# Kernel optimization log

Measured on AMD Instinct MI355X. Metric: run time of the kernel, lower is better.

The kernel has to match this reference:

```python
import jax, jax.numpy as jnp
import numpy as np

N = 8192
HID = 64
TAU = 0.8
LAMBDA = 0.5
POS_DENSITY = 0.005


def setup_inputs() -> dict:
    key = jax.random.key(0)
    k1, k2, k3, k4, k5, k6, k7 = jax.random.split(key, 7)
    x1 = jax.random.normal(k1, (N, HID), dtype=jnp.float32)
    x2 = jax.random.normal(k2, (N, HID), dtype=jnp.float32)
    # xavier_uniform with gain=1.414 for square [HID, HID] linears
    limit = 1.414 * np.sqrt(6.0 / (HID + HID))
    W1 = jax.random.uniform(k3, (HID, HID), dtype=jnp.float32, minval=-limit, maxval=limit)
    b1 = jnp.zeros((HID,), dtype=jnp.float32)
    W2 = jax.random.uniform(k4, (HID, HID), dtype=jnp.float32, minval=-limit, maxval=limit)
    b2 = jnp.zeros((HID,), dtype=jnp.float32)
    pm = (jax.random.uniform(k5, (N, N), dtype=jnp.float32) < POS_DENSITY).astype(jnp.float32)
    positive_matrix = jnp.maximum(pm, jnp.eye(N, dtype=jnp.float32))
    return {"x1": x1, "x2": x2, "W1": W1, "b1": b1, "W2": W2, "b2": b2,
            "positive_matrix": positive_matrix}


def _project(x, W1, b1, W2, b2):
    # nn.Linear(hidden, hidden) -> ELU -> nn.Linear(hidden, hidden)
    h = jax.nn.elu(x @ W1.T + b1)
    return h @ W2.T + b2


def _l2norm(z, eps=1e-12):
    # F.normalize(p=2, dim=1): x / max(||x||, eps)
    n = jnp.linalg.norm(z, axis=-1, keepdims=True)
    return z / jnp.maximum(n, eps)


def _sim(z1, z2, tau):
    return jnp.exp((_l2norm(z1) @ _l2norm(z2).T) / tau)  # [N, N]


def _masked_loss(sim_mat, pos):
    row = sim_mat / (jnp.sum(sim_mat, axis=-1, keepdims=True) + 1e-8)
    return -jnp.log(jnp.sum(row * pos, axis=-1) + 1e-8).mean()


def reference(x1, x2, W1, b1, W2, b2, positive_matrix):
    z1 = _project(x1, W1, b1, W2, b2)
    z2 = _project(x2, W1, b1, W2, b2)
    sc_mp = _sim(z1, z2, TAU)
    mp_sc = _sim(z2, z1, TAU)
    sc_loss = _masked_loss(sc_mp, positive_matrix)
    mp_loss = _masked_loss(mp_sc, positive_matrix)
    return sc_loss * LAMBDA + mp_loss * (1.0 - LAMBDA)
```

## Files before the change

kernel.cpp:

```cpp
#include <hip/hip_runtime.h>
#include <hip/hip_bf16.h>

#define N 8192
#define HID 64
#define JC 8

typedef __attribute__((ext_vector_type(4))) float f32x4;
typedef __attribute__((ext_vector_type(8))) __bf16 bf16x8;

__device__ __forceinline__ void gload_lds16(const void* g, float* l) {
  __builtin_amdgcn_global_load_lds(
      (const __attribute__((address_space(1))) void*)g,
      (__attribute__((address_space(3))) void*)l, 16, 0, 0);
}

__global__ __launch_bounds__(256) void proj_kernel(
    const float* __restrict__ x1, const float* __restrict__ x2,
    const float* __restrict__ W1, const float* __restrict__ b1,
    const float* __restrict__ W2, const float* __restrict__ b2,
    __bf16* __restrict__ Z1h, __bf16* __restrict__ Z2h,
    float* __restrict__ stats)
{
  __shared__ __align__(16) float w1s[64*68];
  __shared__ __align__(16) float w2s[64*68];
  __shared__ __align__(16) float xs[4][64];
  __shared__ __align__(16) float hs[4][64];

  const int tid  = threadIdx.x;
  const int lane = tid & 63;
  const int w    = tid >> 6;

  int gtid = blockIdx.x * 256 + tid;
  if (gtid < 4*N) stats[gtid] = 0.f;

  for (int idx = tid; idx < 64*64; idx += 256) {
    int j = idx >> 6, k = idx & 63;
    w1s[j*68+k] = W1[idx];
    w2s[j*68+k] = W2[idx];
  }
  __syncthreads();

  const float bias1 = b1[lane];
  const float bias2 = b2[lane];

  const int wave_global = blockIdx.x * 4 + w;
  #pragma unroll 1
  for (int it = 0; it < 4; ++it) {
    int R = wave_global * 4 + it;
    const float* src; __bf16* dst;
    if (R < N) { src = x1 + (size_t)R*HID;      dst = Z1h + (size_t)R*HID; }
    else       { src = x2 + (size_t)(R-N)*HID;  dst = Z2h + (size_t)(R-N)*HID; }

    float xv = src[lane];
    xs[w][lane] = xv;
    float acc = bias1;
    #pragma unroll
    for (int qq = 0; qq < 16; ++qq) {
      f32x4 xq = *(const f32x4*)&xs[w][qq*4];
      f32x4 wq = *(const f32x4*)&w1s[lane*68 + qq*4];
      acc += xq.x*wq.x + xq.y*wq.y + xq.z*wq.z + xq.w*wq.w;
    }
    float h = acc > 0.f ? acc : expm1f(acc);
    hs[w][lane] = h;
    float acc2 = bias2;
    #pragma unroll
    for (int qq = 0; qq < 16; ++qq) {
      f32x4 hq = *(const f32x4*)&hs[w][qq*4];
      f32x4 wq = *(const f32x4*)&w2s[lane*68 + qq*4];
      acc2 += hq.x*wq.x + hq.y*wq.y + hq.z*wq.z + hq.w*wq.w;
    }
    float z = acc2;
    float ss = z*z;
    #pragma unroll
    for (int m = 1; m < 64; m <<= 1) ss += __shfl_xor(ss, m);
    float inv = 1.0f / fmaxf(sqrtf(ss), 1e-12f);
    dst[lane] = (__bf16)(z * inv);
  }
}

__global__ __launch_bounds__(256, 4) void sim_kernel(
    const __bf16* __restrict__ Z1h, const __bf16* __restrict__ Z2h,
    const float* __restrict__ pos,
    float* __restrict__ rowsum1, float* __restrict__ num1,
    float* __restrict__ rowsum2, float* __restrict__ num2)
{
  __shared__ __align__(16) float zs1[2][2048];
  __shared__ __align__(16) float zs2[2][2048];

  const int tid  = threadIdx.x;
  const int lane = tid & 63;
  const int w    = tid >> 6;
  const int r16  = lane & 15;
  const int q    = lane >> 4;

  const int bi  = blockIdx.x / JC;
  const int jc  = blockIdx.x % JC;
  const int i0  = bi*64 + w*16;

  const __bf16* z1r = Z1h + (size_t)(i0 + r16)*HID + q*8;
  const __bf16* z2r = Z2h + (size_t)(i0 + r16)*HID + q*8;
  const bf16x8 a1lo = *(const bf16x8*)(z1r);
  const bf16x8 a1hi = *(const bf16x8*)(z1r + 32);
  const bf16x8 a2lo = *(const bf16x8*)(z2r);
  const bf16x8 a2hi = *(const bf16x8*)(z2r + 32);

  float s1 = 0.f, n1 = 0.f, s2 = 0.f, n2 = 0.f;

  const int jbeg = jc * (N/JC);
  const float Cexp = 1.8033688011112042f;
  const float* prow = pos + (size_t)(i0 + r16)*N + q*4;

  f32x4 PA0, PA1, PA2, PA3, PB0, PB1, PB2, PB3;

#define STAGEZ(BUF, JJ) { \
    const int r8 = lane >> 3; \
    const int sl = (lane & 7) ^ r8; \
    gload_lds16(Z1h + (size_t)((JJ) + w*16     + r8)*HID + sl*8, &zs1[BUF][(w*16    )*32]); \
    gload_lds16(Z1h + (size_t)((JJ) + w*16 + 8 + r8)*HID + sl*8, &zs1[BUF][(w*16 + 8)*32]); \
    gload_lds16(Z2h + (size_t)((JJ) + w*16     + r8)*HID + sl*8, &zs2[BUF][(w*16    )*32]); \
    gload_lds16(Z2h + (size_t)((JJ) + w*16 + 8 + r8)*HID + sl*8, &zs2[BUF][(w*16 + 8)*32]); \
  }

#define LOADPOS(P, JJ) { \
    P##0 = *(const f32x4*)(prow + (JJ)); \
    P##1 = *(const f32x4*)(prow + (JJ) + 16); \
    P##2 = *(const f32x4*)(prow + (JJ) + 32); \
    P##3 = *(const f32x4*)(prow + (JJ) + 48); \
  }

#define COMPC(BUF, C, CC, PV) { \
    const int R  = (CC) + (C)*16 + r16; \
    const int sw = r16 & 7; \
    bf16x8 b2lo = *(const bf16x8*)&zs2[BUF][R*32 + ((q    ) ^ sw)*4]; \
    bf16x8 b2hi = *(const bf16x8*)&zs2[BUF][R*32 + ((q + 4) ^ sw)*4]; \
    bf16x8 b1lo = *(const bf16x8*)&zs1[BUF][R*32 + ((q    ) ^ sw)*4]; \
    bf16x8 b1hi = *(const bf16x8*)&zs1[BUF][R*32 + ((q + 4) ^ sw)*4]; \
    f32x4 zero4 = {0.f,0.f,0.f,0.f}; \
    f32x4 d1 = __builtin_amdgcn_mfma_f32_16x16x32_bf16(b2lo, a1lo, zero4, 0,0,0); \
    d1       = __builtin_amdgcn_mfma_f32_16x16x32_bf16(b2hi, a1hi, d1,    0,0,0); \
    f32x4 d2 = __builtin_amdgcn_mfma_f32_16x16x32_bf16(b1lo, a2lo, zero4, 0,0,0); \
    d2       = __builtin_amdgcn_mfma_f32_16x16x32_bf16(b1hi, a2hi, d2,    0,0,0); \
    _Pragma("unroll") \
    for (int r = 0; r < 4; ++r) { \
      float e1 = exp2f(d1[r] * Cexp); \
      float e2 = exp2f(d2[r] * Cexp); \
      s1 += e1; n1 += e1 * PV[r]; \
      s2 += e2; n2 += e2 * PV[r]; \
    } }

#define STEP(BUF, P) { COMPC(BUF,0,0,P##0) COMPC(BUF,1,0,P##1) COMPC(BUF,0,32,P##2) COMPC(BUF,1,32,P##3) }

  STAGEZ(0, jbeg)
  LOADPOS(PA, jbeg)
  __syncthreads();

  #pragma unroll 1
  for (int tp = 0; tp < 7; ++tp) {
    const int t0 = tp*2;
    STAGEZ(1, jbeg + (t0+1)*64)
    LOADPOS(PB, jbeg + (t0+1)*64)
    STEP(0, PA)
    __syncthreads();
    STAGEZ(0, jbeg + (t0+2)*64)
    LOADPOS(PA, jbeg + (t0+2)*64)
    STEP(1, PB)
    __syncthreads();
  }
  STAGEZ(1, jbeg + 15*64)
  LOADPOS(PB, jbeg + 15*64)
  STEP(0, PA)
  __syncthreads();
  STEP(1, PB)

#undef STAGEZ
#undef LOADPOS
#undef COMPC
#undef STEP

  s1 += __shfl_xor(s1, 16); s1 += __shfl_xor(s1, 32);
  n1 += __shfl_xor(n1, 16); n1 += __shfl_xor(n1, 32);
  s2 += __shfl_xor(s2, 16); s2 += __shfl_xor(s2, 32);
  n2 += __shfl_xor(n2, 16); n2 += __shfl_xor(n2, 32);

  if (lane < 16) {
    int row = i0 + r16;
    atomicAdd(&rowsum1[row], s1);
    atomicAdd(&num1[row],    n1);
    atomicAdd(&rowsum2[row], s2);
    atomicAdd(&num2[row],    n2);
  }
}

__global__ __launch_bounds__(1024) void loss_kernel(
    const float* __restrict__ rowsum1, const float* __restrict__ num1,
    const float* __restrict__ rowsum2, const float* __restrict__ num2,
    float* __restrict__ out)
{
  __shared__ float part[16];
  const int tid = threadIdx.x, lane = tid & 63, w = tid >> 6;
  float acc = 0.f;
  for (int i = tid; i < N; i += 1024) {
    float sc = -logf(num1[i]/(rowsum1[i]+1e-8f) + 1e-8f);
    float mp = -logf(num2[i]/(rowsum2[i]+1e-8f) + 1e-8f);
    acc += 0.5f*sc + 0.5f*mp;
  }
  #pragma unroll
  for (int m = 1; m < 64; m <<= 1) acc += __shfl_xor(acc, m);
  if (lane == 0) part[w] = acc;
  __syncthreads();
  if (tid == 0) {
    float t = 0.f;
    #pragma unroll
    for (int k = 0; k < 16; ++k) t += part[k];
    out[0] = t * (1.0f/N);
  }
}

extern "C" void kernel_launch(void* const* d_in, const int* in_sizes, int n_in,
                              void* d_out, int out_size, void* d_ws, size_t ws_size,
                              hipStream_t stream) {
  const float* x1  = (const float*)d_in[0];
  const float* x2  = (const float*)d_in[1];
  const float* W1  = (const float*)d_in[2];
  const float* b1  = (const float*)d_in[3];
  const float* W2  = (const float*)d_in[4];
  const float* b2  = (const float*)d_in[5];
  const float* pos = (const float*)d_in[6];

  char* ws = (char*)d_ws;
  __bf16* Z1h = (__bf16*)ws;
  __bf16* Z2h = (__bf16*)(ws + (size_t)N*HID*sizeof(__bf16));
  size_t zbytes = (size_t)2*N*HID*sizeof(__bf16);
  float* rowsum1 = (float*)(ws + zbytes);
  float* num1    = rowsum1 + N;
  float* rowsum2 = num1 + N;
  float* num2    = rowsum2 + N;

  proj_kernel<<<1024, 256, 0, stream>>>(x1, x2, W1, b1, W2, b2, Z1h, Z2h, rowsum1);
  sim_kernel<<<128*JC, 256, 0, stream>>>(Z1h, Z2h, pos, rowsum1, num1, rowsum2, num2);
  loss_kernel<<<1, 1024, 0, stream>>>(rowsum1, num1, rowsum2, num2, (float*)d_out);
}
```

Measured before the change: 419.0 us.

## Prefetch positive-mask tiles two steps ahead with partial vmcnt waits

Adds a third register set for positive-mask values so mask loads are issued two tiles ahead instead of one. It rotates the buffers through a 6-phase unrolled loop. It replaces __syncthreads with s_waitcnt vmcnt(4) plus s_barrier, so only the older LDS staging loads must complete before the barrier and newer mask loads stay in flight. This aims to hide more of the mask-read latency, the dominant memory stream. The cost is more register pressure, and correctness now depends on the exact order in which memory operations are issued.

```diff
diff --git a/kernel.cpp b/kernel.cpp
--- a/kernel.cpp
+++ b/kernel.cpp
@@ -110,7 +110,7 @@
   const float Cexp = 1.8033688011112042f;
   const float* prow = pos + (size_t)(i0 + r16)*N + q*4;
 
-  f32x4 PA0, PA1, PA2, PA3, PB0, PB1, PB2, PB3;
+  f32x4 PA0, PA1, PA2, PA3, PB0, PB1, PB2, PB3, PC0, PC1, PC2, PC3;
 
 #define STAGEZ(BUF, JJ) { \
     const int r8 = lane >> 3; \
@@ -150,32 +150,43 @@
 
 #define STEP(BUF, P) { COMPC(BUF,0,0,P##0) COMPC(BUF,1,0,P##1) COMPC(BUF,0,32,P##2) COMPC(BUF,1,32,P##3) }
 
+#define PHASE(TB, TBN, PLOAD, PCONS, TT) { \
+    STAGEZ(TBN, jbeg + ((TT)+1)*64) \
+    LOADPOS(PLOAD, jbeg + ((TT)+2)*64) \
+    STEP(TB, PCONS) \
+    asm volatile("s_waitcnt vmcnt(4)" ::: "memory"); \
+    __builtin_amdgcn_s_barrier(); \
+  }
+
   STAGEZ(0, jbeg)
   LOADPOS(PA, jbeg)
-  __syncthreads();
+  LOADPOS(PB, jbeg + 64)
+  asm volatile("s_waitcnt vmcnt(4)" ::: "memory");
+  __builtin_amdgcn_s_barrier();
 
   #pragma unroll 1
-  for (int tp = 0; tp < 7; ++tp) {
-    const int t0 = tp*2;
-    STAGEZ(1, jbeg + (t0+1)*64)
-    LOADPOS(PB, jbeg + (t0+1)*64)
-    STEP(0, PA)
-    __syncthreads();
-    STAGEZ(0, jbeg + (t0+2)*64)
-    LOADPOS(PA, jbeg + (t0+2)*64)
-    STEP(1, PB)
-    __syncthreads();
-  }
+  for (int g = 0; g < 2; ++g) {
+    const int t0 = g*6;
+    PHASE(0, 1, PC, PA, t0+0)
+    PHASE(1, 0, PA, PB, t0+1)
+    PHASE(0, 1, PB, PC, t0+2)
+    PHASE(1, 0, PC, PA, t0+3)
+    PHASE(0, 1, PA, PB, t0+4)
+    PHASE(1, 0, PB, PC, t0+5)
+  }
+  PHASE(0, 1, PC, PA, 12)
+  PHASE(1, 0, PA, PB, 13)
   STAGEZ(1, jbeg + 15*64)
-  LOADPOS(PB, jbeg + 15*64)
-  STEP(0, PA)
-  __syncthreads();
-  STEP(1, PB)
+  STEP(0, PC)
+  asm volatile("s_waitcnt vmcnt(0)" ::: "memory");
+  __builtin_amdgcn_s_barrier();
+  STEP(1, PA)
 
 #undef STAGEZ
 #undef LOADPOS
 #undef COMPC
 #undef STEP
+#undef PHASE
 
   s1 += __shfl_xor(s1, 16); s1 += __shfl_xor(s1, 32);
   n1 += __shfl_xor(n1, 16); n1 += __shfl_xor(n1, 32);
```

After: 422.9 us. About the same (+0.9%).
